# Kernel tuning notes

Hardware: AMD Instinct MI355X
Metric: run time of the kernel (lower is better)

The kernel has to match this reference:

```python
import jax, jax.numpy as jnp
import numpy as np
import math

MIN_NORM = 1e-15
PROJ_EPS = 4e-3  # float32 boundary eps used by HGCN PoincareBall
C = 1.0          # curvature


def _artanh(x):
    return jnp.arctanh(jnp.clip(x, -1.0 + 1e-7, 1.0 - 1e-7))


def proj(x, c):
    norm = jnp.maximum(jnp.linalg.norm(x, axis=-1, keepdims=True), MIN_NORM)
    maxnorm = (1.0 - PROJ_EPS) / jnp.sqrt(c)
    return jnp.where(norm > maxnorm, x / norm * maxnorm, x)


def lambda_x(x, c):
    x2 = jnp.sum(x * x, axis=-1, keepdims=True)
    return 2.0 / jnp.maximum(1.0 - c * x2, MIN_NORM)


def mobius_add(x, y, c):
    x2 = jnp.sum(x * x, axis=-1, keepdims=True)
    y2 = jnp.sum(y * y, axis=-1, keepdims=True)
    xy = jnp.sum(x * y, axis=-1, keepdims=True)
    num = (1.0 + 2.0 * c * xy + c * y2) * x + (1.0 - c * x2) * y
    denom = 1.0 + 2.0 * c * xy + (c ** 2) * x2 * y2
    return num / jnp.maximum(denom, MIN_NORM)


def logmap0(p, c):
    sqrt_c = jnp.sqrt(c)
    p_norm = jnp.maximum(jnp.linalg.norm(p, axis=-1, keepdims=True), MIN_NORM)
    return _artanh(sqrt_c * p_norm) * p / (p_norm * sqrt_c)


def logmap(p1, p2, c):
    # tangent vector at p1 pointing to p2
    sub = mobius_add(-p1, p2, c)
    sub_norm = jnp.maximum(jnp.linalg.norm(sub, axis=-1, keepdims=True), MIN_NORM)
    lam = lambda_x(p1, c)
    sqrt_c = jnp.sqrt(c)
    return 2.0 / (sqrt_c * lam) * _artanh(sqrt_c * sub_norm) * sub / sub_norm


def expmap(u, p, c):
    # exp map of tangent u at base point p
    sqrt_c = jnp.sqrt(c)
    u_norm = jnp.maximum(jnp.linalg.norm(u, axis=-1, keepdims=True), MIN_NORM)
    second = jnp.tanh(sqrt_c / 2.0 * lambda_x(p, c) * u_norm) * u / (sqrt_c * u_norm)
    return mobius_add(p, second, c)


def setup_inputs() -> dict:
    key = jax.random.key(0)
    k1, k2, k3 = jax.random.split(key, 3)
    N, D = 768, 128
    x = jax.random.normal(k1, (N, D), jnp.float32) * 0.1
    x = proj(x, C)  # valid points on the Poincare ball
    adj = (jax.random.uniform(k2, (N, N), jnp.float32) < 0.04).astype(jnp.float32)
    att_w = jax.random.normal(k3, (2 * D, 1), jnp.float32) * (1.0 / math.sqrt(2 * D))
    att_b = jnp.zeros((1,), jnp.float32)
    return {"x": x, "adj": adj, "att_w": att_w, "att_b": att_b}


def reference(x, adj, att_w, att_b):
    c = C
    D = x.shape[-1]
    x_tangent = logmap0(x, c)                               # [N, D]
    # pairwise logmap: tangent at x_i pointing to x_j -> [N, N, D]
    x_local_tangent = logmap(x[:, None, :], x[None, :, :], c)
    # DenseAtt: sigmoid(Linear([xt_i ; xt_j])) * adj, factorized to avoid [N,N,2D]
    s_left = x_tangent @ att_w[:D, 0]                        # [N]
    s_right = x_tangent @ att_w[D:, 0]                       # [N]
    adj_att = jax.nn.sigmoid(s_left[:, None] + s_right[None, :] + att_b[0]) * adj
    support_t = jnp.einsum('ij,ijd->id', adj_att, x_local_tangent)  # [N, D]
    output = proj(expmap(support_t, x, c), c)
    return output
```

## Files before the change

### kernel.cpp

```cpp
#include <hip/hip_runtime.h>
#include <math.h>

#define NN 768
#define DD 128

__device__ __forceinline__ double wred_d(double v) {
    #pragma unroll
    for (int o = 32; o > 0; o >>= 1) v += __shfl_down(v, o, 64);
    return v;
}
__device__ __forceinline__ float wred_f(float v) {
    #pragma unroll
    for (int o = 32; o > 0; o >>= 1) v += __shfl_down(v, o, 64);
    return v;
}

__global__ __launch_bounds__(256) void hypagg_fused(
        const float* __restrict__ x,
        const float* __restrict__ adj,
        const float* __restrict__ att_w,
        const float* __restrict__ att_b,
        float* __restrict__ out) {
    __shared__ float xi[DD];
    __shared__ float wr[DD];
    __shared__ int   list[NN];
    __shared__ float aval[NN];
    __shared__ float dots[NN];
    __shared__ float y2s[NN];
    __shared__ float rds[NN];
    __shared__ float bco[NN];
    __shared__ int   counter;
    __shared__ double pre[2][2];
    __shared__ double s_x2i, s_beta, s_sLi, s_b0;
    __shared__ double cpart[4];
    __shared__ double epart[2][3];

    const int i = blockIdx.x, t = threadIdx.x;
    const int wid = t >> 6, lane = t & 63;

    float xv = 0.0f;
    if (t < DD) {
        xv = x[i * DD + t];
        xi[t] = xv;
        wr[t] = att_w[DD + t];
        double dx2 = wred_d((double)xv * xv);
        double dwl = wred_d((double)xv * (double)att_w[t]);
        if (lane == 0) { pre[wid][0] = dx2; pre[wid][1] = dwl; }
    }
    if (t == 0) counter = 0;
    __syncthreads();

    if (t == 0) {
        double x2 = pre[0][0] + pre[1][0];
        double dl = pre[0][1] + pre[1][1];
        double r  = sqrt(x2);
        double g0 = atanh(fmin(r, 1.0 - 1e-7)) / fmax(r, 1e-15);
        s_x2i = x2;
        s_beta = 1.0 - x2;
        s_sLi = g0 * dl;
        s_b0  = (double)att_b[0];
    }

    for (int j = t; j < NN; j += 256) {
        float a = adj[i * NN + j];
        if (a != 0.0f) {
            int k = atomicAdd(&counter, 1);
            list[k] = j;
            aval[k] = a;
        }
    }
    __syncthreads();
    const int n = counter;

    for (int k = wid; k < n; k += 4) {
        const float* xj = x + (size_t)list[k] * DD;
        float a0 = xj[lane], a1 = xj[lane + 64];
        double dd = wred_d((double)xi[lane] * a0 + (double)xi[lane + 64] * a1);
        double dy = wred_d((double)a0 * a0 + (double)a1 * a1);
        float  dr = wred_f(wr[lane] * a0 + wr[lane + 64] * a1);
        if (lane == 0) { dots[k] = (float)dd; y2s[k] = (float)dy; rds[k] = dr; }
    }
    __syncthreads();

    double asum = 0.0;
    {
        const double x2i = s_x2i, beta = s_beta, sLi = s_sLi, b0 = s_b0;
        const double factor = fmax(beta, 1e-15);
        for (int k = t; k < n; k += 256) {
            double dot = (double)dots[k];
            double y2  = (double)y2s[k];
            double ry  = sqrt(y2);
            double g0j = atanh(fmin(ry, 1.0 - 1e-7)) / fmax(ry, 1e-15);
            double z   = sLi + g0j * (double)rds[k] + b0;
            double w   = (double)aval[k] / (1.0 + exp(-z));
            double alpha  = 1.0 - 2.0 * dot + y2;
            double denomc = fmax(1.0 - 2.0 * dot + x2i * y2, 1e-15);
            double sn2 = (alpha * alpha * x2i - 2.0 * alpha * beta * dot + beta * beta * y2)
                         / (denomc * denomc);
            double sn  = fmax(sqrt(fmax(sn2, 0.0)), 1e-15);
            double g   = atanh(fmin(sn, 1.0 - 1e-7)) / sn;
            double common = w * factor * g / denomc;
            asum -= common * alpha;
            bco[k] = (float)(common * beta);
        }
    }
    asum = wred_d(asum);
    if (lane == 0) cpart[wid] = asum;
    __syncthreads();

    double u = 0.0;
    if (t < DD) {
        const double rowA = cpart[0] + cpart[1] + cpart[2] + cpart[3];
        u = rowA * (double)xv;
        for (int k = 0; k < n; ++k)
            u += (double)bco[k] * (double)x[(size_t)list[k] * DD + t];
        double p_un2 = wred_d(u * u);
        double p_xu  = wred_d((double)xv * u);
        if (lane == 0) { epart[wid][0] = p_un2; epart[wid][1] = p_xu; }
    }
    __syncthreads();

    double ov = 0.0;
    if (t < DD) {
        double un2 = epart[0][0] + epart[1][0];
        double xu  = epart[0][1] + epart[1][1];
        double lamfac = fmax(s_beta, 1e-15);
        double un = fmax(sqrt(un2), 1e-15);
        double th = tanh(un / lamfac);
        double s  = th / un;
        double y2 = s * s * un2;
        double xy = s * xu;
        double c1 = 1.0 + 2.0 * xy + y2;
        double c2 = 1.0 - s_x2i;
        double den = fmax(1.0 + 2.0 * xy + s_x2i * y2, 1e-15);
        ov = (c1 * (double)xv + c2 * s * u) / den;
        double p_on2 = wred_d(ov * ov);
        if (lane == 0) epart[wid][2] = p_on2;
    }
    __syncthreads();

    if (t < DD) {
        double on2 = epart[0][2] + epart[1][2];
        double on  = fmax(sqrt(on2), 1e-15);
        const double maxn = 1.0 - 4e-3;
        double scale = (on > maxn) ? (maxn / on) : 1.0;
        out[i * DD + t] = (float)(ov * scale);
    }
}

extern "C" void kernel_launch(void* const* d_in, const int* in_sizes, int n_in,
                              void* d_out, int out_size, void* d_ws, size_t ws_size,
                              hipStream_t stream) {
    const float* x     = (const float*)d_in[0];
    const float* adj   = (const float*)d_in[1];
    const float* att_w = (const float*)d_in[2];
    const float* att_b = (const float*)d_in[3];
    float* out = (float*)d_out;
    hypagg_fused<<<NN, 256, 0, stream>>>(x, adj, att_w, att_b, out);
}
```

Before: 78.47 us.

## Cache neighbor rows in LDS, vectorize adjacency scan and row loads

Neighbor rows of x fetched during the dot-product pass are stored in a 64-row shared-memory cache, so the later weighted aggregation reads them from LDS instead of global memory. The adjacency scan now uses float4 loads with one atomic per thread, and neighbor row loads use float2. The cache adds 32 KB of shared memory per block, which may reduce occupancy.

Result: no change. 77.72 us (-1.0%).

```diff
diff --git a/kernel.cpp b/kernel.cpp
--- a/kernel.cpp
+++ b/kernel.cpp
@@ -3,6 +3,7 @@
 
 #define NN 768
 #define DD 128
+#define XC 64
 
 __device__ __forceinline__ double wred_d(double v) {
     #pragma unroll
@@ -23,6 +24,7 @@
         float* __restrict__ out) {
     __shared__ float xi[DD];
     __shared__ float wr[DD];
+    __shared__ float xcache[XC][DD];
     __shared__ int   list[NN];
     __shared__ float aval[NN];
     __shared__ float dots[NN];
@@ -61,23 +63,32 @@
         s_b0  = (double)att_b[0];
     }
 
-    for (int j = t; j < NN; j += 256) {
-        float a = adj[i * NN + j];
-        if (a != 0.0f) {
-            int k = atomicAdd(&counter, 1);
-            list[k] = j;
-            aval[k] = a;
+    if (t < NN / 4) {
+        float4 a = ((const float4*)(adj + (size_t)i * NN))[t];
+        int m = (a.x != 0.0f) + (a.y != 0.0f) + (a.z != 0.0f) + (a.w != 0.0f);
+        if (m) {
+            int base = atomicAdd(&counter, m);
+            int j = 4 * t;
+            if (a.x != 0.0f) { list[base] = j;     aval[base] = a.x; ++base; }
+            if (a.y != 0.0f) { list[base] = j + 1; aval[base] = a.y; ++base; }
+            if (a.z != 0.0f) { list[base] = j + 2; aval[base] = a.z; ++base; }
+            if (a.w != 0.0f) { list[base] = j + 3; aval[base] = a.w; ++base; }
         }
     }
     __syncthreads();
     const int n = counter;
 
+    const float2* xi2 = (const float2*)xi;
+    const float2* wr2 = (const float2*)wr;
     for (int k = wid; k < n; k += 4) {
-        const float* xj = x + (size_t)list[k] * DD;
-        float a0 = xj[lane], a1 = xj[lane + 64];
-        double dd = wred_d((double)xi[lane] * a0 + (double)xi[lane + 64] * a1);
-        double dy = wred_d((double)a0 * a0 + (double)a1 * a1);
-        float  dr = wred_f(wr[lane] * a0 + wr[lane + 64] * a1);
+        const float2* xj2 = (const float2*)(x + (size_t)list[k] * DD);
+        float2 a  = xj2[lane];
+        if (k < XC) ((float2*)xcache[k])[lane] = a;
+        float2 xw = xi2[lane];
+        float2 ww = wr2[lane];
+        double dd = wred_d((double)xw.x * a.x + (double)xw.y * a.y);
+        double dy = wred_d((double)a.x * a.x + (double)a.y * a.y);
+        float  dr = wred_f(ww.x * a.x + ww.y * a.y);
         if (lane == 0) { dots[k] = (float)dd; y2s[k] = (float)dy; rds[k] = dr; }
     }
     __syncthreads();
@@ -112,7 +123,10 @@
     if (t < DD) {
         const double rowA = cpart[0] + cpart[1] + cpart[2] + cpart[3];
         u = rowA * (double)xv;
-        for (int k = 0; k < n; ++k)
+        const int nc = (n < XC) ? n : XC;
+        for (int k = 0; k < nc; ++k)
+            u += (double)bco[k] * (double)xcache[k][t];
+        for (int k = XC; k < n; ++k)
             u += (double)bco[k] * (double)x[(size_t)list[k] * DD + t];
         double p_un2 = wred_d(u * u);
         double p_xu  = wred_d((double)xv * u);
```
